# Performance work log

Hardware: AMD Instinct MI355X
Metric: run time of the kernel (lower is better)

The kernel has to match this reference:

```python
import jax, jax.numpy as jnp
import numpy as np

IGNORE_INDEX = -100


def setup_inputs() -> dict:
    key = jax.random.key(0)
    k1, k2, k3 = jax.random.split(key, 3)
    N, H, V = 4096, 2048, 50257
    x = jax.random.normal(k1, (N, H), dtype=jnp.float32)
    weight = jax.random.normal(k2, (V, H), dtype=jnp.float32) * (1.0 / np.sqrt(H))
    y = jax.random.randint(k3, (N,), 0, V, dtype=jnp.int64)
    return {"x": x, "weight": weight, "y": y}


def reference(x, weight, y):
    # Fused linear + cross entropy: logits = x @ W^T, mean NLL over non-ignored tokens.
    logits = jnp.einsum("nh,vh->nv", x, weight)  # [N, V]
    logp = jax.nn.log_softmax(logits, axis=-1)
    mask = (y != IGNORE_INDEX)
    safe_y = jnp.where(mask, y, 0)
    nll = -jnp.take_along_axis(logp, safe_y[:, None], axis=-1)[:, 0]  # [N]
    n_valid = jnp.maximum(jnp.sum(mask), 1)
    loss = jnp.sum(jnp.where(mask, nll, 0.0)) / n_valid.astype(nll.dtype)
    return loss
```

## Files before the change

### kernel.cpp

```cpp
#include <hip/hip_runtime.h>
#include <hip/hip_bf16.h>
#include <math.h>

typedef unsigned char  u8;
typedef unsigned int   u32;
typedef __attribute__((ext_vector_type(8)))  int   int8v;
typedef __attribute__((ext_vector_type(16))) float f32x16;

typedef __attribute__((address_space(3))) void lds_void;
typedef __attribute__((address_space(1))) void gbl_void;

#define IGNORE_INDEX (-100)

__device__ __forceinline__ u8 f32_to_e4m3(float f) {
    union { float f; u32 u; } v; v.f = f;
    u32 s  = (v.u >> 24) & 0x80u;
    u32 au = v.u & 0x7FFFFFFFu;
    float a = __uint_as_float(au);
    if (a >= 448.0f) return (u8)(s | 0x7E);
    int e = (int)(au >> 23) - 127;
    if (e >= -6) {
        u32 m    = au & 0x7FFFFFu;
        u32 keep = m >> 20;
        u32 rest = m & 0xFFFFFu;
        keep += (rest > 0x80000u) || (rest == 0x80000u && (keep & 1u));
        u32 code = ((u32)(e + 7) << 3) + keep;
        if (code > 0x7E) code = 0x7E;
        return (u8)(s | code);
    } else {
        int q = (int)rintf(a * 512.0f);
        return (u8)(s | (u32)q);
    }
}

__global__ __launch_bounds__(256) void cvt_pack_fp8(const float* __restrict__ in,
                                                    u8* __restrict__ out,
                                                    float scale, int H, int nRows) {
    __shared__ __align__(16) u8 lds[16384];
    const int kc    = blockIdx.x;
    const int panel = blockIdx.y;
    const int t     = threadIdx.x;

#pragma unroll
    for (int it = 0; it < 4; ++it) {
        int u  = it * 256 + t;
        int r  = u >> 3;
        int cc = u & 7;
        int row = panel * 128 + r;
        u8 tmp[16];
        if (row < nRows) {
            const float* src = in + (size_t)row * H + kc * 128 + cc * 16;
#pragma unroll
            for (int p = 0; p < 4; ++p) {
                float4 f = *(const float4*)(src + p * 4);
                tmp[p * 4 + 0] = f32_to_e4m3(f.x * scale);
                tmp[p * 4 + 1] = f32_to_e4m3(f.y * scale);
                tmp[p * 4 + 2] = f32_to_e4m3(f.z * scale);
                tmp[p * 4 + 3] = f32_to_e4m3(f.w * scale);
            }
        } else {
#pragma unroll
            for (int p = 0; p < 16; ++p) tmp[p] = 0;
        }
        int i2 = r >> 5, ln32 = r & 31;
        int ks = cc >> 2, khalf = (cc >> 1) & 1, h = cc & 1;
        int s  = i2 * 4 + ks * 2 + h;
        int lane = khalf * 32 + ln32;
        *(int4*)(lds + s * 1024 + lane * 16) = *(const int4*)tmp;
    }
    __syncthreads();

    u8* dst = out + ((size_t)panel * gridDim.x + kc) * 16384;
    const int4* l4 = (const int4*)lds;
    int4* d4 = (int4*)dst;
#pragma unroll
    for (int p = 0; p < 4; ++p)
        d4[p * 256 + t] = l4[p * 256 + t];
}

__global__ __launch_bounds__(256) void gemm_lse_partial(
    const u8* __restrict__ Ap,
    const u8* __restrict__ Bp,
    float2* __restrict__ partials,
    int KC, int V, int VT)
{
    __shared__ __align__(16) u8 As[16 * 1024];
    __shared__ __align__(16) u8 Bs[16 * 1024];

    const int tid  = threadIdx.x;
    const int w    = tid >> 6;
    const int lane = tid & 63;
    const int wm   = w >> 1, wn = w & 1;
    const int ln32 = lane & 31;
    const int khalf = lane >> 5;

    const int mBase = blockIdx.x * 128;
    const int vTile = blockIdx.y;
    const int vBase = vTile * 128;

    f32x16 acc[2][2];
#pragma unroll
    for (int i = 0; i < 2; ++i)
#pragma unroll
        for (int j = 0; j < 2; ++j)
#pragma unroll
            for (int r = 0; r < 16; ++r) acc[i][j][r] = 0.0f;

    const int scaleA = 0x7C7C7C7C;
    const int scaleB = 0x7B7B7B7B;

    const u8* aSrc = Ap + ((size_t)blockIdx.x * KC) * 16384 + (w * 4096 + lane * 16);
    const u8* bSrc = Bp + ((size_t)vTile      * KC) * 16384 + (w * 4096 + lane * 16);
    u8* aDst = (u8*)As + w * 4096;
    u8* bDst = (u8*)Bs + w * 4096;

    const u8* aRd = As + lane * 16;
    const u8* bRd = Bs + lane * 16;

    for (int kc = 0; kc < KC; ++kc) {
        __builtin_amdgcn_global_load_lds((gbl_void*)(aSrc       ), (lds_void*)(aDst       ), 16, 0, 0);
        __builtin_amdgcn_global_load_lds((gbl_void*)(aSrc + 1024), (lds_void*)(aDst + 1024), 16, 0, 0);
        __builtin_amdgcn_global_load_lds((gbl_void*)(aSrc + 2048), (lds_void*)(aDst + 2048), 16, 0, 0);
        __builtin_amdgcn_global_load_lds((gbl_void*)(aSrc + 3072), (lds_void*)(aDst + 3072), 16, 0, 0);
        __builtin_amdgcn_global_load_lds((gbl_void*)(bSrc       ), (lds_void*)(bDst       ), 16, 0, 0);
        __builtin_amdgcn_global_load_lds((gbl_void*)(bSrc + 1024), (lds_void*)(bDst + 1024), 16, 0, 0);
        __builtin_amdgcn_global_load_lds((gbl_void*)(bSrc + 2048), (lds_void*)(bDst + 2048), 16, 0, 0);
        __builtin_amdgcn_global_load_lds((gbl_void*)(bSrc + 3072), (lds_void*)(bDst + 3072), 16, 0, 0);
        aSrc += 16384; bSrc += 16384;
        __syncthreads();

#pragma unroll
        for (int ks = 0; ks < 2; ++ks) {
            int8v af[2], bf[2];
#pragma unroll
            for (int i = 0; i < 2; ++i) {
                int sA = ((wm * 2 + i) * 4 + ks * 2) * 1024;
                int4 lo = *(const int4*)(aRd + sA);
                int4 hi = *(const int4*)(aRd + sA + 1024);
                int8v a; a[0]=lo.x; a[1]=lo.y; a[2]=lo.z; a[3]=lo.w;
                         a[4]=hi.x; a[5]=hi.y; a[6]=hi.z; a[7]=hi.w;
                af[i] = a;
                int sB = ((wn * 2 + i) * 4 + ks * 2) * 1024;
                lo = *(const int4*)(bRd + sB);
                hi = *(const int4*)(bRd + sB + 1024);
                int8v b; b[0]=lo.x; b[1]=lo.y; b[2]=lo.z; b[3]=lo.w;
                         b[4]=hi.x; b[5]=hi.y; b[6]=hi.z; b[7]=hi.w;
                bf[i] = b;
            }
#pragma unroll
            for (int i = 0; i < 2; ++i)
#pragma unroll
                for (int j = 0; j < 2; ++j)
                    acc[i][j] = __builtin_amdgcn_mfma_scale_f32_32x32x64_f8f6f4(
                        af[i], bf[j], acc[i][j], 0, 0, 0, scaleA, 0, scaleB);
        }
        __syncthreads();
    }

    bool vj[2];
#pragma unroll
    for (int j = 0; j < 2; ++j)
        vj[j] = (vBase + wn * 64 + j * 32 + ln32) < V;

    float2* red = (float2*)As;

#pragma unroll
    for (int i = 0; i < 2; ++i) {
#pragma unroll
        for (int r = 0; r < 16; ++r) {
            float v0 = vj[0] ? acc[i][0][r] : -INFINITY;
            float v1 = vj[1] ? acc[i][1][r] : -INFINITY;
            float m = fmaxf(v0, v1);
#pragma unroll
            for (int o = 1; o < 32; o <<= 1)
                m = fmaxf(m, __shfl_xor(m, o, 64));
            float s = 0.0f;
            if (vj[0]) s += __expf(acc[i][0][r] - m);
            if (vj[1]) s += __expf(acc[i][1][r] - m);
#pragma unroll
            for (int o = 1; o < 32; o <<= 1)
                s += __shfl_xor(s, o, 64);
            if (ln32 == 0) {
                int row = wm * 64 + i * 32 + (r & 3) + 8 * (r >> 2) + 4 * khalf;
                red[row * 2 + wn] = make_float2(m, s);
            }
        }
    }
    __syncthreads();

    if (tid < 128) {
        float2 p0 = red[tid * 2 + 0];
        float2 p1 = red[tid * 2 + 1];
        float m = fmaxf(p0.x, p1.x);
        float s = p0.y * __expf(p0.x - m) + p1.y * __expf(p1.x - m);
        partials[(size_t)(mBase + tid) * VT + vTile] = make_float2(m, s);
    }
}

__global__ __launch_bounds__(256) void row_final(
    const float* __restrict__ x,
    const float* __restrict__ W,
    const int* __restrict__ y,
    const float2* __restrict__ partials,
    float* __restrict__ nll, float* __restrict__ valid,
    int H, int V, int VT)
{
    const int n = blockIdx.x;
    const int t = threadIdx.x;
    const int yn = y[n];
    const bool ok = (yn != IGNORE_INDEX);

    float dsum = 0.0f;
    if (ok) {
        int cy = yn; if (cy < 0) cy = 0; if (cy >= V) cy = V - 1;
        const float4* xr = (const float4*)(x + (size_t)n * H);
        const float4* wr = (const float4*)(W + (size_t)cy * H);
        int nf4 = H >> 2;
        for (int i = t; i < nf4; i += 256) {
            float4 a = xr[i], b = wr[i];
            dsum += a.x * b.x + a.y * b.y + a.z * b.z + a.w * b.w;
        }
    }

    float m = -INFINITY, s = 0.0f;
    const float2* pr = partials + (size_t)n * VT;
    for (int i = t; i < VT; i += 256) {
        float2 p = pr[i];
        float nm = fmaxf(m, p.x);
        s = s * __expf(m - nm) + p.y * __expf(p.x - nm);
        m = nm;
    }

    __shared__ float rm[256], rs[256], rd[256];
    rm[t] = m; rs[t] = s; rd[t] = dsum;
    __syncthreads();
    for (int o = 128; o > 0; o >>= 1) {
        if (t < o) {
            float m2 = rm[t + o], s2 = rs[t + o];
            float nm = fmaxf(rm[t], m2);
            rs[t] = rs[t] * __expf(rm[t] - nm) + s2 * __expf(m2 - nm);
            rm[t] = nm;
            rd[t] += rd[t + o];
        }
        __syncthreads();
    }
    if (t == 0) {
        float lse = rm[0] + __logf(rs[0]);
        nll[n]   = ok ? (lse - rd[0]) : 0.0f;
        valid[n] = ok ? 1.0f : 0.0f;
    }
}

__global__ __launch_bounds__(1024) void final_loss(
    const float* __restrict__ nll, const float* __restrict__ valid,
    float* __restrict__ out, int n)
{
    __shared__ float ss[1024], sv[1024];
    const int t = threadIdx.x;
    float a = 0.0f, b = 0.0f;
    for (int i = t; i < n; i += 1024) { a += nll[i]; b += valid[i]; }
    ss[t] = a; sv[t] = b;
    __syncthreads();
    for (int o = 512; o > 0; o >>= 1) {
        if (t < o) { ss[t] += ss[t + o]; sv[t] += sv[t + o]; }
        __syncthreads();
    }
    if (t == 0) out[0] = ss[0] / fmaxf(sv[0], 1.0f);
}

extern "C" void kernel_launch(void* const* d_in, const int* in_sizes, int n_in,
                              void* d_out, int out_size, void* d_ws, size_t ws_size,
                              hipStream_t stream) {
    const float* x = (const float*)d_in[0];
    const float* W = (const float*)d_in[1];
    const int*   y = (const int*)d_in[2];

    const long xsz = in_sizes[0];
    const long wsz = in_sizes[1];
    const int  N   = in_sizes[2];
    const int  H   = (int)(xsz / N);
    const int  V   = (int)(wsz / H);
    const int  VT  = (V + 127) / 128;
    const int  MT  = N / 128;
    const int  KC  = H / 128;

    char* ws = (char*)d_ws;
    size_t off = 0;
    u8* Wp = (u8*)(ws + off); off += (size_t)VT * KC * 16384; off = (off + 255) & ~(size_t)255;
    u8* Xp = (u8*)(ws + off); off += (size_t)MT * KC * 16384; off = (off + 255) & ~(size_t)255;
    float2* partials = (float2*)(ws + off); off += (size_t)N * VT * sizeof(float2); off = (off + 255) & ~(size_t)255;
    float* nll   = (float*)(ws + off); off += (size_t)N * 4;
    float* valid = (float*)(ws + off); off += (size_t)N * 4;

    cvt_pack_fp8<<<dim3(KC, VT), 256, 0, stream>>>(W, Wp, 16.0f, H, V);
    cvt_pack_fp8<<<dim3(KC, MT), 256, 0, stream>>>(x, Xp, 8.0f, H, N);

    dim3 grid(MT, VT);
    gemm_lse_partial<<<grid, 256, 0, stream>>>(Xp, Wp, partials, KC, V, VT);

    row_final<<<N, 256, 0, stream>>>(x, W, y, partials, nll, valid, H, V, VT);
    final_loss<<<1, 1024, 0, stream>>>(nll, valid, (float*)d_out, N);
}
```

Baseline: 1.229 ms.

## Load prepacked MFMA fragments directly from global memory, dropping LDS staging

The GEMM main loop no longer stages A and B tiles through shared memory with global_load_lds and barriers. Each wave loads its own prepacked fp8 fragments straight from global memory into registers, and the loop is unrolled by two. This removes per-chunk barriers and LDS traffic and frees LDS for higher occupancy. In exchange, tiles shared between waves are fetched twice from global/L2, and load latency is no longer hidden by cooperative staging.

New measurement: 1.209 ms. Within noise of the previous version (-1.7%).

```diff
diff --git a/kernel.cpp b/kernel.cpp
--- a/kernel.cpp
+++ b/kernel.cpp
@@ -6,9 +6,6 @@
 typedef unsigned int   u32;
 typedef __attribute__((ext_vector_type(8)))  int   int8v;
 typedef __attribute__((ext_vector_type(16))) float f32x16;
-
-typedef __attribute__((address_space(3))) void lds_void;
-typedef __attribute__((address_space(1))) void gbl_void;
 
 #define IGNORE_INDEX (-100)
 
@@ -78,14 +75,19 @@
         d4[p * 256 + t] = l4[p * 256 + t];
 }
 
+#define LD8(dst, base, off) { \
+    int4 lo_ = *(const int4*)((base) + (off)); \
+    int4 hi_ = *(const int4*)((base) + (off) + 1024); \
+    dst[0]=lo_.x; dst[1]=lo_.y; dst[2]=lo_.z; dst[3]=lo_.w; \
+    dst[4]=hi_.x; dst[5]=hi_.y; dst[6]=hi_.z; dst[7]=hi_.w; }
+
 __global__ __launch_bounds__(256) void gemm_lse_partial(
     const u8* __restrict__ Ap,
     const u8* __restrict__ Bp,
     float2* __restrict__ partials,
     int KC, int V, int VT)
 {
-    __shared__ __align__(16) u8 As[16 * 1024];
-    __shared__ __align__(16) u8 Bs[16 * 1024];
+    __shared__ float2 red[256];
 
     const int tid  = threadIdx.x;
     const int w    = tid >> 6;
@@ -109,60 +111,38 @@
     const int scaleA = 0x7C7C7C7C;
     const int scaleB = 0x7B7B7B7B;
 
-    const u8* aSrc = Ap + ((size_t)blockIdx.x * KC) * 16384 + (w * 4096 + lane * 16);
-    const u8* bSrc = Bp + ((size_t)vTile      * KC) * 16384 + (w * 4096 + lane * 16);
-    u8* aDst = (u8*)As + w * 4096;
-    u8* bDst = (u8*)Bs + w * 4096;
-
-    const u8* aRd = As + lane * 16;
-    const u8* bRd = Bs + lane * 16;
-
+    const u8* aPtr = Ap + ((size_t)blockIdx.x * KC) * 16384 + lane * 16;
+    const u8* bPtr = Bp + ((size_t)vTile      * KC) * 16384 + lane * 16;
+
+    const int aO0 = (wm * 2    ) * 4096;
+    const int aO1 = (wm * 2 + 1) * 4096;
+    const int bO0 = (wn * 2    ) * 4096;
+    const int bO1 = (wn * 2 + 1) * 4096;
+
+#pragma unroll 2
     for (int kc = 0; kc < KC; ++kc) {
-        __builtin_amdgcn_global_load_lds((gbl_void*)(aSrc       ), (lds_void*)(aDst       ), 16, 0, 0);
-        __builtin_amdgcn_global_load_lds((gbl_void*)(aSrc + 1024), (lds_void*)(aDst + 1024), 16, 0, 0);
-        __builtin_amdgcn_global_load_lds((gbl_void*)(aSrc + 2048), (lds_void*)(aDst + 2048), 16, 0, 0);
-        __builtin_amdgcn_global_load_lds((gbl_void*)(aSrc + 3072), (lds_void*)(aDst + 3072), 16, 0, 0);
-        __builtin_amdgcn_global_load_lds((gbl_void*)(bSrc       ), (lds_void*)(bDst       ), 16, 0, 0);
-        __builtin_amdgcn_global_load_lds((gbl_void*)(bSrc + 1024), (lds_void*)(bDst + 1024), 16, 0, 0);
-        __builtin_amdgcn_global_load_lds((gbl_void*)(bSrc + 2048), (lds_void*)(bDst + 2048), 16, 0, 0);
-        __builtin_amdgcn_global_load_lds((gbl_void*)(bSrc + 3072), (lds_void*)(bDst + 3072), 16, 0, 0);
-        aSrc += 16384; bSrc += 16384;
-        __syncthreads();
-
-#pragma unroll
-        for (int ks = 0; ks < 2; ++ks) {
-            int8v af[2], bf[2];
-#pragma unroll
-            for (int i = 0; i < 2; ++i) {
-                int sA = ((wm * 2 + i) * 4 + ks * 2) * 1024;
-                int4 lo = *(const int4*)(aRd + sA);
-                int4 hi = *(const int4*)(aRd + sA + 1024);
-                int8v a; a[0]=lo.x; a[1]=lo.y; a[2]=lo.z; a[3]=lo.w;
-                         a[4]=hi.x; a[5]=hi.y; a[6]=hi.z; a[7]=hi.w;
-                af[i] = a;
-                int sB = ((wn * 2 + i) * 4 + ks * 2) * 1024;
-                lo = *(const int4*)(bRd + sB);
-                hi = *(const int4*)(bRd + sB + 1024);
-                int8v b; b[0]=lo.x; b[1]=lo.y; b[2]=lo.z; b[3]=lo.w;
-                         b[4]=hi.x; b[5]=hi.y; b[6]=hi.z; b[7]=hi.w;
-                bf[i] = b;
-            }
-#pragma unroll
-            for (int i = 0; i < 2; ++i)
-#pragma unroll
-                for (int j = 0; j < 2; ++j)
-                    acc[i][j] = __builtin_amdgcn_mfma_scale_f32_32x32x64_f8f6f4(
-                        af[i], bf[j], acc[i][j], 0, 0, 0, scaleA, 0, scaleB);
-        }
-        __syncthreads();
+        int8v a00, a10, b00, b10, a01, a11, b01, b11;
+        LD8(a00, aPtr, aO0);           LD8(a10, aPtr, aO1);
+        LD8(b00, bPtr, bO0);           LD8(b10, bPtr, bO1);
+        LD8(a01, aPtr, aO0 + 2048);    LD8(a11, aPtr, aO1 + 2048);
+        LD8(b01, bPtr, bO0 + 2048);    LD8(b11, bPtr, bO1 + 2048);
+
+        acc[0][0] = __builtin_amdgcn_mfma_scale_f32_32x32x64_f8f6f4(a00, b00, acc[0][0], 0, 0, 0, scaleA, 0, scaleB);
+        acc[0][1] = __builtin_amdgcn_mfma_scale_f32_32x32x64_f8f6f4(a00, b10, acc[0][1], 0, 0, 0, scaleA, 0, scaleB);
+        acc[1][0] = __builtin_amdgcn_mfma_scale_f32_32x32x64_f8f6f4(a10, b00, acc[1][0], 0, 0, 0, scaleA, 0, scaleB);
+        acc[1][1] = __builtin_amdgcn_mfma_scale_f32_32x32x64_f8f6f4(a10, b10, acc[1][1], 0, 0, 0, scaleA, 0, scaleB);
+        acc[0][0] = __builtin_amdgcn_mfma_scale_f32_32x32x64_f8f6f4(a01, b01, acc[0][0], 0, 0, 0, scaleA, 0, scaleB);
+        acc[0][1] = __builtin_amdgcn_mfma_scale_f32_32x32x64_f8f6f4(a01, b11, acc[0][1], 0, 0, 0, scaleA, 0, scaleB);
+        acc[1][0] = __builtin_amdgcn_mfma_scale_f32_32x32x64_f8f6f4(a11, b01, acc[1][0], 0, 0, 0, scaleA, 0, scaleB);
+        acc[1][1] = __builtin_amdgcn_mfma_scale_f32_32x32x64_f8f6f4(a11, b11, acc[1][1], 0, 0, 0, scaleA, 0, scaleB);
+
+        aPtr += 16384; bPtr += 16384;
     }
 
     bool vj[2];
 #pragma unroll
     for (int j = 0; j < 2; ++j)
         vj[j] = (vBase + wn * 64 + j * 32 + ln32) < V;
-
-    float2* red = (float2*)As;
 
 #pragma unroll
     for (int i = 0; i < 2; ++i) {
```
